# Optimization experiments

Measured on AMD Instinct MI355X. Metric: run time of the kernel, lower is better.

Reference implementation:

```python
import jax, jax.numpy as jnp
import numpy as np

EPS = 1e-6

def rmsnorm(x, scale):
    return x * jax.lax.rsqrt(jnp.mean(x * x, axis=-1, keepdims=True) + EPS) * scale

def setup_inputs() -> dict:
    key = jax.random.key(0)
    ks = jax.random.split(key, 8)
    B1, B2 = 16, 64
    D, H, A = 8192, 1024, 2          # deter_size, hidden_size, action_size
    S, C, G = 32, 64, 8              # stoch_size, classes, blocks
    sc = 0.02                        # trunc-normal-ish init scale
    f32 = jnp.float32
    return dict(
        deter=jax.random.normal(ks[0], (B1, B2, D), f32),
        stoch=jax.random.normal(ks[1], (B1, B2, S, C), f32),
        action=jax.random.normal(ks[2], (B1, B2, A), f32),
        W1=(jax.random.normal(ks[3], (H, D), f32) * sc),
        b1=jnp.zeros((H,), f32),
        s1=jnp.ones((H,), f32),
        W2=(jax.random.normal(ks[4], (H, S * C), f32) * sc),
        b2=jnp.zeros((H,), f32),
        s2=jnp.ones((H,), f32),
        W3=(jax.random.normal(ks[5], (H, A), f32) * sc),
        b3=jnp.zeros((H,), f32),
        s3=jnp.ones((H,), f32),
        Wb1=(jax.random.normal(ks[6], (G, (3 * G * H + D) // G, D // G), f32) * sc),
        bb1=jnp.zeros((D,), f32),
        sb1=jnp.ones((D,), f32),
        Wb2=(jax.random.normal(ks[7], (G, D // G, 3 * D // G), f32) * sc),
        bb2=jnp.zeros((3 * D,), f32),
    )

def reference(deter, stoch, action, W1, b1, s1, W2, b2, s2, W3, b3, s3, Wb1, bb1, sb1, Wb2, bb2):
    batch_shape = deter.shape[:-1]
    D = deter.shape[-1]
    d = deter.reshape(-1, D)                       # (B, D)
    B = d.shape[0]
    G = Wb1.shape[0]
    H = W1.shape[0]
    s = stoch.reshape(B, -1)                       # (B, S*C)
    a = action.reshape(B, -1)                      # (B, A)
    a = a / jax.lax.stop_gradient(jnp.maximum(1.0, jnp.abs(a)))
    # three parallel Linear + RMSNorm + SiLU branches
    x1 = jax.nn.silu(rmsnorm(d @ W1.T + b1, s1))
    x2 = jax.nn.silu(rmsnorm(s @ W2.T + b2, s2))
    x3 = jax.nn.silu(rmsnorm(a @ W3.T + b3, s3))
    x = jnp.concatenate([x1, x2, x3], axis=-1)     # (B, 3H)
    x = jnp.broadcast_to(x[:, None, :], (B, G, 3 * H))
    x = jnp.concatenate([x, d.reshape(B, G, D // G)], axis=-1)  # (B, G, 3H + D/G)
    # block-diagonal grouped GEMM + RMSNorm + SiLU (dyn_layers=1)
    h = jnp.einsum('bgi,gio->bgo', x, Wb1).reshape(B, D) + bb1
    h = jax.nn.silu(rmsnorm(h, sb1))
    # final block-diagonal GEMM -> 3*D gate pre-activations
    y = jnp.einsum('bgi,gio->bgo', h.reshape(B, G, D // G), Wb2).reshape(B, 3 * D) + bb2
    r, c, u = jnp.split(y.reshape(B, G, -1), 3, axis=-1)        # each (B, G, D/G)
    reset = jax.nn.sigmoid(r.reshape(B, D))
    cand = jnp.tanh(reset * c.reshape(B, D))
    update = jax.nn.sigmoid(u.reshape(B, D) - 1.0)
    next_deter = update * cand + (1.0 - update) * d
    return next_deter.reshape(*batch_shape, D)
```

## Files before the change

### kernel.cpp

```cpp
#include <hip/hip_runtime.h>
#include <stdint.h>

typedef unsigned short ushort_t;
typedef __attribute__((ext_vector_type(8))) short bf16x8;
typedef __attribute__((ext_vector_type(4))) float f32x4;

#define EPS 1e-6f

__device__ __forceinline__ float b2f(ushort_t u) {
    union { uint32_t i; float f; } v; v.i = ((uint32_t)u) << 16; return v.f;
}
__device__ __forceinline__ ushort_t f2b(float f) {
    union { float f; uint32_t i; } v; v.f = f;
    uint32_t x = v.i;
    uint32_t r = (x + 0x7fffu + ((x >> 16) & 1u)) >> 16;
    return (ushort_t)r;
}

__device__ __forceinline__ void async_copy16(const void* g, void* l) {
    __builtin_amdgcn_global_load_lds(
        (const __attribute__((address_space(1))) uint32_t*)(uintptr_t)g,
        (__attribute__((address_space(3))) uint32_t*)(uintptr_t)l,
        16, 0, 0);
}

__global__ __launch_bounds__(256) void cast4_k(
    const float* __restrict__ s0, ushort_t* __restrict__ d0, int n0,
    const float* __restrict__ s1, ushort_t* __restrict__ d1, int n1,
    const float* __restrict__ s2, ushort_t* __restrict__ d2, int n2,
    const float* __restrict__ s3, ushort_t* __restrict__ d3) {
    int j = blockIdx.x * 256 + threadIdx.x;
    const float* s; ushort_t* d;
    if (j < n0) { s = s0; d = d0; }
    else if ((j -= n0) < n1) { s = s1; d = d1; }
    else if ((j -= n1) < n2) { s = s2; d = d2; }
    else { j -= n2; s = s3; d = d3; }
    float4 v = ((const float4*)s)[j];
    ushort4 o;
    o.x = f2b(v.x); o.y = f2b(v.y); o.z = f2b(v.z); o.w = f2b(v.w);
    ((ushort4*)d)[j] = o;
}

__global__ __launch_bounds__(256) void transpose_cast_k(const float* __restrict__ src,
                                                        ushort_t* __restrict__ dst,
                                                        int R, int C) {
    __shared__ float tile[32][33];
    int bat = blockIdx.z;
    int c0 = blockIdx.x * 32, r0 = blockIdx.y * 32;
    const float* s = src + (size_t)bat * R * C;
    ushort_t* d = dst + (size_t)bat * R * C;
    int tx = threadIdx.x, ty = threadIdx.y;
    float4 v = *(const float4*)&s[(size_t)(r0 + ty) * C + c0 + tx * 4];
    tile[ty][tx * 4 + 0] = v.x;
    tile[ty][tx * 4 + 1] = v.y;
    tile[ty][tx * 4 + 2] = v.z;
    tile[ty][tx * 4 + 3] = v.w;
    __syncthreads();
    ushort4 o;
    o.x = f2b(tile[tx * 4 + 0][ty]);
    o.y = f2b(tile[tx * 4 + 1][ty]);
    o.z = f2b(tile[tx * 4 + 2][ty]);
    o.w = f2b(tile[tx * 4 + 3][ty]);
    *(ushort4*)&d[(size_t)(c0 + ty) * R + r0 + tx * 4] = o;
}

template <int MODE, bool OUT_BF16>
__global__ __launch_bounds__(256) void gemm_bt_k(
    const ushort_t* __restrict__ Aa, const ushort_t* __restrict__ Ab,
    const ushort_t* __restrict__ Bw,
    float* __restrict__ Cf, ushort_t* __restrict__ Cb,
    int lda, int ldb, int ldc, int Ksl, int k0base, int czoff) {
    __shared__ __align__(16) ushort_t As[2][64 * 64];
    __shared__ __align__(16) ushort_t Bs[2][128 * 64];
    const int tid = threadIdx.x;

    const int gx = gridDim.x;
    const int nxy = gx * gridDim.y;
    const int flat = blockIdx.x + blockIdx.y * gx;
    const int cpx = nxy >> 3;
    const int L = (flat & 7) * cpx + (flat >> 3);
    const int bm = L % gx, bn = L / gx;
    const int bz = blockIdx.z;
    const int k0 = k0base + bz * Ksl;
    const int m0 = bm * 64, n0 = bn * 128;
    const int cz = bz * czoff;
    const int lane = tid & 63, w = tid >> 6;
    const int wm = (w & 1) * 32, wn = (w >> 1) * 64;

    f32x4 acc[2][4];
#pragma unroll
    for (int i = 0; i < 2; i++)
#pragma unroll
        for (int j = 0; j < 4; j++) acc[i][j] = (f32x4){0.f, 0.f, 0.f, 0.f};

    auto a_ptr = [&](int m, int kk) -> const ushort_t* {
        if (MODE == 0) {
            return Aa + (size_t)m * lda + kk;
        } else if (MODE == 1) {
            if (kk < 3072) return Aa + (size_t)m * 3072 + kk;
            int g = n0 >> 10;
            return Ab + (size_t)m * 8192 + g * 1024 + (kk - 3072);
        } else {
            int g = n0 / 3072;
            return Aa + (size_t)m * 8192 + g * 1024 + kk;
        }
    };

    const int srow = tid >> 3;
    const int sslot = tid & 7;
    const int gco = (sslot ^ (srow & 7)) << 3;
    const int lco = sslot << 3;

    auto stage = [&](int buf, int kk) {
#pragma unroll
        for (int p = 0; p < 2; ++p) {
            int r = (p << 5) + srow;
            async_copy16(a_ptr(m0 + r, kk + gco), &As[buf][r * 64 + lco]);
        }
#pragma unroll
        for (int p = 0; p < 4; ++p) {
            int r = (p << 5) + srow;
            async_copy16(Bw + (size_t)(n0 + r) * ldb + kk + gco, &Bs[buf][r * 64 + lco]);
        }
    };

    const int nt = Ksl >> 6;
    stage(0, k0);
    __builtin_amdgcn_sched_barrier(0);

    const int qc = lane >> 4;
    const int rl = lane & 15;
    int cur = 0;

    for (int t = 0; t < nt; ++t) {
        if (t + 1 < nt) {
            stage(cur ^ 1, k0 + ((t + 1) << 6));
            asm volatile("s_waitcnt vmcnt(6)" ::: "memory");
        } else {
            asm volatile("s_waitcnt vmcnt(0)" ::: "memory");
        }
        __builtin_amdgcn_s_barrier();
        __builtin_amdgcn_sched_barrier(0);

#pragma unroll
        for (int h = 0; h < 2; ++h) {
            bf16x8 af[2], bfr[4];
#pragma unroll
            for (int i = 0; i < 2; i++) {
                int ra = wm + i * 16 + rl;
                int slot = ((h << 2) + qc) ^ (ra & 7);
                af[i] = *(const bf16x8*)&As[cur][ra * 64 + (slot << 3)];
            }
#pragma unroll
            for (int j = 0; j < 4; j++) {
                int rb = wn + j * 16 + rl;
                int slot = ((h << 2) + qc) ^ (rb & 7);
                bfr[j] = *(const bf16x8*)&Bs[cur][rb * 64 + (slot << 3)];
            }
#pragma unroll
            for (int i = 0; i < 2; i++)
#pragma unroll
                for (int j = 0; j < 4; j++)
                    acc[i][j] = __builtin_amdgcn_mfma_f32_16x16x32_bf16(af[i], bfr[j], acc[i][j], 0, 0, 0);
        }

        if (t + 1 < nt) {
            __builtin_amdgcn_sched_barrier(0);
            __builtin_amdgcn_s_barrier();
            __builtin_amdgcn_sched_barrier(0);
            cur ^= 1;
        }
    }

    const int cr = (lane >> 4) * 4, cc = lane & 15;
#pragma unroll
    for (int i = 0; i < 2; i++) {
#pragma unroll
        for (int j = 0; j < 4; j++) {
#pragma unroll
            for (int r = 0; r < 4; r++) {
                int row = m0 + wm + i * 16 + cr + r;
                int col = n0 + cz + wn + j * 16 + cc;
                float v = acc[i][j][r];
                if (OUT_BF16) {
                    Cb[(size_t)row * ldc + col] = f2b(v);
                } else {
                    Cf[(size_t)row * ldc + col] = v;
                }
            }
        }
    }
}

__global__ __launch_bounds__(256) void branch3_k(const float* __restrict__ act,
                                                 const float* __restrict__ W3,
                                                 float* __restrict__ xacc) {
    int idx = blockIdx.x * 256 + threadIdx.x;
    int b = idx >> 10, h = idx & 1023;
    float a0 = act[b * 2 + 0], a1 = act[b * 2 + 1];
    a0 = a0 / fmaxf(1.f, fabsf(a0));
    a1 = a1 / fmaxf(1.f, fabsf(a1));
    float v = a0 * W3[h * 2 + 0] + a1 * W3[h * 2 + 1];
    xacc[(size_t)b * 7168 + 6144 + h] = v;
}

__global__ __launch_bounds__(256) void norm_silu_1024_k(
    const float* __restrict__ xacc,
    const float* __restrict__ b1, const float* __restrict__ s1,
    const float* __restrict__ b2, const float* __restrict__ s2,
    const float* __restrict__ b3, const float* __restrict__ s3,
    ushort_t* __restrict__ xbf) {
    int b = blockIdx.x, c = blockIdx.y, tid = threadIdx.x;
    const float* bias = (c == 0) ? b1 : (c == 1) ? b2 : b3;
    const float* scl  = (c == 0) ? s1 : (c == 1) ? s2 : s3;
    const float* row = xacc + (size_t)b * 7168 + ((c == 0) ? 0 : (c == 1) ? 4096 : 6144);
    const int np = (c == 0) ? 4 : (c == 1) ? 2 : 1;
    float4 v = ((const float4*)row)[tid];
#pragma unroll 4
    for (int p = 1; p < np; ++p) {
        float4 t = ((const float4*)(row + p * 1024))[tid];
        v.x += t.x; v.y += t.y; v.z += t.z; v.w += t.w;
    }
    float4 bb = ((const float4*)bias)[tid];
    v.x += bb.x; v.y += bb.y; v.z += bb.z; v.w += bb.w;
    float ss = v.x * v.x + v.y * v.y + v.z * v.z + v.w * v.w;
#pragma unroll
    for (int off = 32; off > 0; off >>= 1) ss += __shfl_down(ss, off, 64);
    __shared__ float wsum[4];
    int lane = tid & 63, wid = tid >> 6;
    if (lane == 0) wsum[wid] = ss;
    __syncthreads();
    float tot = wsum[0] + wsum[1] + wsum[2] + wsum[3];
    float rms = rsqrtf(tot * (1.0f / 1024.0f) + EPS);
    float4 sc = ((const float4*)scl)[tid];
    float o0 = v.x * rms * sc.x; o0 = o0 / (1.f + __expf(-o0));
    float o1 = v.y * rms * sc.y; o1 = o1 / (1.f + __expf(-o1));
    float o2 = v.z * rms * sc.z; o2 = o2 / (1.f + __expf(-o2));
    float o3 = v.w * rms * sc.w; o3 = o3 / (1.f + __expf(-o3));
    ushort4 o; o.x = f2b(o0); o.y = f2b(o1); o.z = f2b(o2); o.w = f2b(o3);
    ((ushort4*)(xbf + (size_t)b * 3072 + c * 1024))[tid] = o;
}

__global__ __launch_bounds__(256) void norm_silu_8192_k(const float* __restrict__ hpre,
                                                        const float* __restrict__ bb1,
                                                        const float* __restrict__ sb1,
                                                        ushort_t* __restrict__ hbf) {
    int b = blockIdx.x, tid = threadIdx.x;
    const float4* src = (const float4*)(hpre + (size_t)b * 8192);
    float4 v[8];
    float ss = 0.f;
#pragma unroll
    for (int k = 0; k < 8; k++) {
        float4 t = src[tid + k * 256];
        float4 bv = ((const float4*)bb1)[tid + k * 256];
        t.x += bv.x; t.y += bv.y; t.z += bv.z; t.w += bv.w;
        v[k] = t;
        ss += t.x * t.x + t.y * t.y + t.z * t.z + t.w * t.w;
    }
#pragma unroll
    for (int off = 32; off > 0; off >>= 1) ss += __shfl_down(ss, off, 64);
    __shared__ float wsum[4];
    int lane = tid & 63, wid = tid >> 6;
    if (lane == 0) wsum[wid] = ss;
    __syncthreads();
    float tot = wsum[0] + wsum[1] + wsum[2] + wsum[3];
    float rms = rsqrtf(tot * (1.0f / 8192.0f) + EPS);
    ushort_t* dst = hbf + (size_t)b * 8192;
#pragma unroll
    for (int k = 0; k < 8; k++) {
        float4 sv = ((const float4*)sb1)[tid + k * 256];
        float o0 = v[k].x * rms * sv.x; o0 = o0 / (1.f + __expf(-o0));
        float o1 = v[k].y * rms * sv.y; o1 = o1 / (1.f + __expf(-o1));
        float o2 = v[k].z * rms * sv.z; o2 = o2 / (1.f + __expf(-o2));
        float o3 = v[k].w * rms * sv.w; o3 = o3 / (1.f + __expf(-o3));
        ushort4 o; o.x = f2b(o0); o.y = f2b(o1); o.z = f2b(o2); o.w = f2b(o3);
        ((ushort4*)dst)[tid + k * 256] = o;
    }
}

__global__ __launch_bounds__(256) void gates_k(const ushort_t* __restrict__ y,
                                               const float* __restrict__ bb2,
                                               const float* __restrict__ deter,
                                               float* __restrict__ out) {
    int idx = blockIdx.x * 256 + threadIdx.x;
    int f = idx * 4;
    int b = f >> 13, d = f & 8191;
    int g = d >> 10, j = d & 1023;
    size_t ybase = (size_t)b * 24576 + g * 3072 + j;
    ushort4 rv = *(const ushort4*)(y + ybase);
    ushort4 cv = *(const ushort4*)(y + ybase + 1024);
    ushort4 uv = *(const ushort4*)(y + ybase + 2048);
    float4 bbr = *(const float4*)(bb2 + g * 3072 + j);
    float4 bbc = *(const float4*)(bb2 + g * 3072 + 1024 + j);
    float4 bbu = *(const float4*)(bb2 + g * 3072 + 2048 + j);
    float4 dv = *(const float4*)(deter + f);
    float rr[4] = {b2f(rv.x) + bbr.x, b2f(rv.y) + bbr.y, b2f(rv.z) + bbr.z, b2f(rv.w) + bbr.w};
    float cc[4] = {b2f(cv.x) + bbc.x, b2f(cv.y) + bbc.y, b2f(cv.z) + bbc.z, b2f(cv.w) + bbc.w};
    float uu[4] = {b2f(uv.x) + bbu.x, b2f(uv.y) + bbu.y, b2f(uv.z) + bbu.z, b2f(uv.w) + bbu.w};
    float dd[4] = {dv.x, dv.y, dv.z, dv.w};
    float oo[4];
#pragma unroll
    for (int t = 0; t < 4; t++) {
        float reset = 1.f / (1.f + __expf(-rr[t]));
        float cand = tanhf(reset * cc[t]);
        float upd = 1.f / (1.f + __expf(-(uu[t] - 1.f)));
        oo[t] = upd * cand + (1.f - upd) * dd[t];
    }
    float4 o; o.x = oo[0]; o.y = oo[1]; o.z = oo[2]; o.w = oo[3];
    *(float4*)(out + f) = o;
}

extern "C" void kernel_launch(void* const* d_in, const int* in_sizes, int n_in,
                              void* d_out, int out_size, void* d_ws, size_t ws_size,
                              hipStream_t stream) {
    const float* deter = (const float*)d_in[0];
    const float* stoch = (const float*)d_in[1];
    const float* action = (const float*)d_in[2];
    const float* W1 = (const float*)d_in[3];
    const float* b1 = (const float*)d_in[4];
    const float* s1 = (const float*)d_in[5];
    const float* W2 = (const float*)d_in[6];
    const float* b2 = (const float*)d_in[7];
    const float* s2 = (const float*)d_in[8];
    const float* W3 = (const float*)d_in[9];
    const float* b3 = (const float*)d_in[10];
    const float* s3 = (const float*)d_in[11];
    const float* Wb1 = (const float*)d_in[12];
    const float* bb1 = (const float*)d_in[13];
    const float* sb1 = (const float*)d_in[14];
    const float* Wb2 = (const float*)d_in[15];
    const float* bb2 = (const float*)d_in[16];
    float* out = (float*)d_out;

    char* ws = (char*)d_ws;
    ushort_t* dbf  = (ushort_t*)(ws + 0);
    ushort_t* sbf  = (ushort_t*)(ws + 16777216);
    ushort_t* W1bf = (ushort_t*)(ws + 20971520);
    ushort_t* W2bf = (ushort_t*)(ws + 37748736);
    ushort_t* Wb1T = (ushort_t*)(ws + 41943040);
    ushort_t* Wb2T = (ushort_t*)(ws + 109051904);
    ushort_t* xbf  = (ushort_t*)(ws + 171966464);
    float*    hpre = (float*)   (ws + 178257920);
    ushort_t* hbf  = (ushort_t*)(ws + 211812352);
    ushort_t* ybf  = (ushort_t*)(ws + 228589568);
    float*    xacc = hpre;

    cast4_k<<<20480, 256, 0, stream>>>(deter, dbf, 2097152,
                                       stoch, sbf, 524288,
                                       W1, W1bf, 2097152,
                                       W2, W2bf);
    transpose_cast_k<<<dim3(32, 128, 8), dim3(8, 32), 0, stream>>>(Wb1, Wb1T, 4096, 1024);
    transpose_cast_k<<<dim3(96, 32, 8), dim3(8, 32), 0, stream>>>(Wb2, Wb2T, 1024, 3072);

    gemm_bt_k<0, false><<<dim3(16, 8, 4), 256, 0, stream>>>(
        dbf, nullptr, W1bf, xacc, nullptr, 8192, 8192, 7168, 2048, 0, 1024);
    gemm_bt_k<0, false><<<dim3(16, 8, 2), 256, 0, stream>>>(
        sbf, nullptr, W2bf, xacc + 4096, nullptr, 2048, 2048, 7168, 1024, 0, 1024);
    branch3_k<<<4096, 256, 0, stream>>>(action, W3, xacc);

    norm_silu_1024_k<<<dim3(1024, 3), 256, 0, stream>>>(xacc, b1, s1, b2, s2, b3, s3, xbf);

    gemm_bt_k<1, false><<<dim3(16, 64, 1), 256, 0, stream>>>(
        xbf, dbf, Wb1T, hpre, nullptr, 0, 4096, 8192, 4096, 0, 0);

    norm_silu_8192_k<<<1024, 256, 0, stream>>>(hpre, bb1, sb1, hbf);

    gemm_bt_k<2, true><<<dim3(16, 192, 1), 256, 0, stream>>>(
        hbf, nullptr, Wb2T, nullptr, ybf, 0, 1024, 24576, 1024, 0, 0);

    gates_k<<<8192, 256, 0, stream>>>(ybf, bb2, deter, out);
}
```

Measured before the change: 624.2 us.

## Templatize GEMM tile sizes and use larger tiles with split-K for block GEMMs

```diff
diff --git a/kernel.cpp b/kernel.cpp
--- a/kernel.cpp
+++ b/kernel.cpp
@@ -64,14 +64,18 @@
     *(ushort4*)&d[(size_t)(c0 + ty) * R + r0 + tx * 4] = o;
 }
 
-template <int MODE, bool OUT_BF16>
-__global__ __launch_bounds__(256) void gemm_bt_k(
+template <int MODE, bool OUT_BF16, int BM, int BN, int WNW>
+__global__ __launch_bounds__(WNW * 128, 2) void gemm_bt_k(
     const ushort_t* __restrict__ Aa, const ushort_t* __restrict__ Ab,
     const ushort_t* __restrict__ Bw,
     float* __restrict__ Cf, ushort_t* __restrict__ Cb,
     int lda, int ldb, int ldc, int Ksl, int k0base, int czoff) {
-    __shared__ __align__(16) ushort_t As[2][64 * 64];
-    __shared__ __align__(16) ushort_t Bs[2][128 * 64];
+    constexpr int THREADS = WNW * 128;
+    constexpr int MR = (BM / 2) / 16;
+    constexpr int NR = (BN / WNW) / 16;
+    constexpr int SR = THREADS >> 3;
+    __shared__ __align__(16) ushort_t As[2][BM * 64];
+    __shared__ __align__(16) ushort_t Bs[2][BN * 64];
     const int tid = threadIdx.x;
 
     const int gx = gridDim.x;
@@ -82,16 +86,17 @@
     const int bm = L % gx, bn = L / gx;
     const int bz = blockIdx.z;
     const int k0 = k0base + bz * Ksl;
-    const int m0 = bm * 64, n0 = bn * 128;
+    const int m0 = bm * BM, n0 = bn * BN;
     const int cz = bz * czoff;
     const int lane = tid & 63, w = tid >> 6;
-    const int wm = (w & 1) * 32, wn = (w >> 1) * 64;
-
-    f32x4 acc[2][4];
-#pragma unroll
-    for (int i = 0; i < 2; i++)
-#pragma unroll
-        for (int j = 0; j < 4; j++) acc[i][j] = (f32x4){0.f, 0.f, 0.f, 0.f};
+    const int wm = (w & 1) * (BM / 2);
+    const int wn = (w >> 1) * (BN / WNW);
+
+    f32x4 acc[MR][NR];
+#pragma unroll
+    for (int i = 0; i < MR; i++)
+#pragma unroll
+        for (int j = 0; j < NR; j++) acc[i][j] = (f32x4){0.f, 0.f, 0.f, 0.f};
 
     auto a_ptr = [&](int m, int kk) -> const ushort_t* {
         if (MODE == 0) {
@@ -113,13 +118,13 @@
 
     auto stage = [&](int buf, int kk) {
 #pragma unroll
-        for (int p = 0; p < 2; ++p) {
-            int r = (p << 5) + srow;
+        for (int p = 0; p < BM / SR; ++p) {
+            int r = p * SR + srow;
             async_copy16(a_ptr(m0 + r, kk + gco), &As[buf][r * 64 + lco]);
         }
 #pragma unroll
-        for (int p = 0; p < 4; ++p) {
-            int r = (p << 5) + srow;
+        for (int p = 0; p < BN / SR; ++p) {
+            int r = p * SR + srow;
             async_copy16(Bw + (size_t)(n0 + r) * ldb + kk + gco, &Bs[buf][r * 64 + lco]);
         }
     };
@@ -135,7 +140,7 @@
     for (int t = 0; t < nt; ++t) {
         if (t + 1 < nt) {
             stage(cur ^ 1, k0 + ((t + 1) << 6));
-            asm volatile("s_waitcnt vmcnt(6)" ::: "memory");
+            asm volatile("s_waitcnt vmcnt(8)" ::: "memory");
         } else {
             asm volatile("s_waitcnt vmcnt(0)" ::: "memory");
         }
@@ -144,23 +149,23 @@
 
 #pragma unroll
         for (int h = 0; h < 2; ++h) {
-            bf16x8 af[2], bfr[4];
-#pragma unroll
-            for (int i = 0; i < 2; i++) {
+            bf16x8 af[MR], bfr[NR];
+#pragma unroll
+            for (int i = 0; i < MR; i++) {
                 int ra = wm + i * 16 + rl;
                 int slot = ((h << 2) + qc) ^ (ra & 7);
                 af[i] = *(const bf16x8*)&As[cur][ra * 64 + (slot << 3)];
             }
 #pragma unroll
-            for (int j = 0; j < 4; j++) {
+            for (int j = 0; j < NR; j++) {
                 int rb = wn + j * 16 + rl;
                 int slot = ((h << 2) + qc) ^ (rb & 7);
                 bfr[j] = *(const bf16x8*)&Bs[cur][rb * 64 + (slot << 3)];
             }
 #pragma unroll
-            for (int i = 0; i < 2; i++)
-#pragma unroll
-                for (int j = 0; j < 4; j++)
+            for (int i = 0; i < MR; i++)
+#pragma unroll
+                for (int j = 0; j < NR; j++)
                     acc[i][j] = __builtin_amdgcn_mfma_f32_16x16x32_bf16(af[i], bfr[j], acc[i][j], 0, 0, 0);
         }
 
@@ -174,9 +179,9 @@
 
     const int cr = (lane >> 4) * 4, cc = lane & 15;
 #pragma unroll
-    for (int i = 0; i < 2; i++) {
-#pragma unroll
-        for (int j = 0; j < 4; j++) {
+    for (int i = 0; i < MR; i++) {
+#pragma unroll
+        for (int j = 0; j < NR; j++) {
 #pragma unroll
             for (int r = 0; r < 4; r++) {
                 int row = m0 + wm + i * 16 + cr + r;
@@ -246,12 +251,14 @@
                                                         const float* __restrict__ sb1,
                                                         ushort_t* __restrict__ hbf) {
     int b = blockIdx.x, tid = threadIdx.x;
-    const float4* src = (const float4*)(hpre + (size_t)b * 8192);
+    const float4* src = (const float4*)(hpre + (size_t)b * 16384);
     float4 v[8];
     float ss = 0.f;
 #pragma unroll
     for (int k = 0; k < 8; k++) {
         float4 t = src[tid + k * 256];
+        float4 u = src[tid + k * 256 + 2048];
+        t.x += u.x; t.y += u.y; t.z += u.z; t.w += u.w;
         float4 bv = ((const float4*)bb1)[tid + k * 256];
         t.x += bv.x; t.y += bv.y; t.z += bv.z; t.w += bv.w;
         v[k] = t;
@@ -333,17 +340,17 @@
     float* out = (float*)d_out;
 
     char* ws = (char*)d_ws;
-    ushort_t* dbf  = (ushort_t*)(ws + 0);
-    ushort_t* sbf  = (ushort_t*)(ws + 16777216);
-    ushort_t* W1bf = (ushort_t*)(ws + 20971520);
-    ushort_t* W2bf = (ushort_t*)(ws + 37748736);
-    ushort_t* Wb1T = (ushort_t*)(ws + 41943040);
-    ushort_t* Wb2T = (ushort_t*)(ws + 109051904);
-    ushort_t* xbf  = (ushort_t*)(ws + 171966464);
-    float*    hpre = (float*)   (ws + 178257920);
-    ushort_t* hbf  = (ushort_t*)(ws + 211812352);
-    ushort_t* ybf  = (ushort_t*)(ws + 228589568);
-    float*    xacc = hpre;
+    ushort_t* dbf   = (ushort_t*)(ws + 0);
+    ushort_t* sbf   = (ushort_t*)(ws + 16777216);
+    ushort_t* W1bf  = (ushort_t*)(ws + 20971520);
+    ushort_t* W2bf  = (ushort_t*)(ws + 37748736);
+    ushort_t* Wb1T  = (ushort_t*)(ws + 41943040);
+    ushort_t* Wb2T  = (ushort_t*)(ws + 109051904);
+    ushort_t* xbf   = (ushort_t*)(ws + 159383552);
+    float*    hpre2 = (float*)   (ws + 165675008);
+    ushort_t* hbf   = (ushort_t*)(ws + 232783872);
+    float*    xacc = hpre2;
+    ushort_t* ybf  = (ushort_t*)hpre2;
 
     cast4_k<<<20480, 256, 0, stream>>>(deter, dbf, 2097152,
                                        stoch, sbf, 524288,
@@ -352,20 +359,20 @@
     transpose_cast_k<<<dim3(32, 128, 8), dim3(8, 32), 0, stream>>>(Wb1, Wb1T, 4096, 1024);
     transpose_cast_k<<<dim3(96, 32, 8), dim3(8, 32), 0, stream>>>(Wb2, Wb2T, 1024, 3072);
 
-    gemm_bt_k<0, false><<<dim3(16, 8, 4), 256, 0, stream>>>(
+    gemm_bt_k<0, false, 128, 128, 2><<<dim3(8, 8, 4), 256, 0, stream>>>(
         dbf, nullptr, W1bf, xacc, nullptr, 8192, 8192, 7168, 2048, 0, 1024);
-    gemm_bt_k<0, false><<<dim3(16, 8, 2), 256, 0, stream>>>(
+    gemm_bt_k<0, false, 128, 128, 2><<<dim3(8, 8, 2), 256, 0, stream>>>(
         sbf, nullptr, W2bf, xacc + 4096, nullptr, 2048, 2048, 7168, 1024, 0, 1024);
     branch3_k<<<4096, 256, 0, stream>>>(action, W3, xacc);
 
     norm_silu_1024_k<<<dim3(1024, 3), 256, 0, stream>>>(xacc, b1, s1, b2, s2, b3, s3, xbf);
 
-    gemm_bt_k<1, false><<<dim3(16, 64, 1), 256, 0, stream>>>(
-        xbf, dbf, Wb1T, hpre, nullptr, 0, 4096, 8192, 4096, 0, 0);
-
-    norm_silu_8192_k<<<1024, 256, 0, stream>>>(hpre, bb1, sb1, hbf);
-
-    gemm_bt_k<2, true><<<dim3(16, 192, 1), 256, 0, stream>>>(
+    gemm_bt_k<1, false, 256, 256, 4><<<dim3(4, 32, 2), 512, 0, stream>>>(
+        xbf, dbf, Wb1T, hpre2, nullptr, 0, 4096, 16384, 2048, 0, 8192);
+
+    norm_silu_8192_k<<<1024, 256, 0, stream>>>(hpre2, bb1, sb1, hbf);
+
+    gemm_bt_k<2, true, 256, 256, 4><<<dim3(4, 96, 1), 512, 0, stream>>>(
         hbf, nullptr, Wb2T, nullptr, ybf, 0, 1024, 24576, 1024, 0, 0);
 
     gates_k<<<8192, 256, 0, stream>>>(ybf, bb2, deter, out);
```

After: 586.8 us. 6.0% less time.
